# Optimization experiments

Hardware: AMD Instinct MI355X
Metric: run time of the kernel (lower is better)

## Reference

```python
import jax, jax.numpy as jnp
import numpy as np

B, T, C, H, MAX_LEN = 16, 512, 1024, 16, 512
D = C // H  # head_dim = 64

def setup_inputs() -> dict:
    key = jax.random.key(0)
    ks = jax.random.split(key, 10)
    s = 1.0 / np.sqrt(C)
    return {
        "x": jax.random.normal(ks[0], (B, T, C), dtype=jnp.float32),
        "Wq": jax.random.normal(ks[1], (C, C), dtype=jnp.float32) * s,
        "bq": jnp.zeros((C,), dtype=jnp.float32),
        "Wk": jax.random.normal(ks[2], (C, C), dtype=jnp.float32) * s,
        "bk": jnp.zeros((C,), dtype=jnp.float32),
        "Wv": jax.random.normal(ks[3], (C, C), dtype=jnp.float32) * s,
        "bv": jnp.zeros((C,), dtype=jnp.float32),
        "Wo": jax.random.normal(ks[4], (C, C), dtype=jnp.float32) * s,
        "bo": jnp.zeros((C,), dtype=jnp.float32),
        "rel_pos_bias": jax.random.normal(ks[5], (H, MAX_LEN, MAX_LEN), dtype=jnp.float32) * 0.02,
    }

def reference(x, Wq, bq, Wk, bk, Wv, bv, Wo, bo, rel_pos_bias):
    scale = 1.0 / jnp.sqrt(jnp.float32(D))
    # projections (torch Linear: x @ W.T + b), reshape to (B,H,T,D)
    def proj(W, b):
        return (x @ W.T + b).reshape(B, T, H, D).transpose(0, 2, 1, 3)
    q, k, v = proj(Wq, bq), proj(Wk, bk), proj(Wv, bv)
    attn = jnp.einsum('bhtd,bhsd->bhts', q, k) * scale  # (B,H,T,T)
    attn = attn + rel_pos_bias[None, :, :T, :T]
    causal = jnp.triu(jnp.ones((T, T), dtype=bool), k=1)
    attn = jnp.where(causal[None, None], -jnp.inf, attn)
    attn = jax.nn.softmax(attn, axis=-1)  # dropout p=0 (eval) -> identity
    out = jnp.einsum('bhts,bhsd->bhtd', attn, v)
    out = out.transpose(0, 2, 1, 3).reshape(B, T, C)
    return out @ Wo.T + bo
```

## Files before the change

### kernel.cpp

```cpp
#include <hip/hip_runtime.h>
#include <stdint.h>
#include <math.h>

#define DEV static __device__ __forceinline__

typedef __attribute__((ext_vector_type(8))) __bf16 bf16x8;
typedef __attribute__((ext_vector_type(4))) float f32x4;
typedef unsigned short u16;

DEV u16 f2b(float f) {
  union { float f; uint32_t u; } x; x.f = f;
  uint32_t r = x.u + 0x7fffu + ((x.u >> 16) & 1u);
  return (u16)(r >> 16);
}

DEV uint32_t pk2(float a, float b) {
  return (uint32_t)f2b(a) | ((uint32_t)f2b(b) << 16);
}

DEV float b2f_lo(uint32_t u) { return __uint_as_float(u << 16); }
DEV float b2f_hi(uint32_t u) { return __uint_as_float(u & 0xffff0000u); }

DEV void glds16(const void* g, void* l) {
  __builtin_amdgcn_global_load_lds(
      (const __attribute__((address_space(1))) void*)g,
      (__attribute__((address_space(3))) void*)l, 16, 0, 0);
}

DEV f32x4 mfma16(bf16x8 a, bf16x8 b, f32x4 c) {
  return __builtin_amdgcn_mfma_f32_16x16x32_bf16(a, b, c, 0, 0, 0);
}

__global__ __launch_bounds__(256) void cvt_all(
    const float* __restrict__ x, const float* __restrict__ Wq,
    const float* __restrict__ Wk, const float* __restrict__ Wv,
    const float* __restrict__ Wo, const float* __restrict__ bias,
    u16* __restrict__ xb, u16* __restrict__ wqkv, u16* __restrict__ wo,
    u16* __restrict__ biasb) {
  size_t i = ((size_t)blockIdx.x * 256 + threadIdx.x) * 4;
  const float* s;
  u16* d;
  size_t off;
  float scale = 1.0f;
  if (i < 8388608)        { s = x;  d = xb;             off = i; }
  else if (i < 9437184)   { s = Wq; d = wqkv;           off = i - 8388608; }
  else if (i < 10485760)  { s = Wk; d = wqkv + 1048576; off = i - 9437184; }
  else if (i < 11534336)  { s = Wv; d = wqkv + 2097152; off = i - 10485760; }
  else if (i < 12582912)  { s = Wo; d = wo;             off = i - 11534336; }
  else { s = bias; d = biasb; off = i - 12582912; scale = 1.44269504f; }
  float4 v = *(const float4*)(s + off);
  ushort4 o;
  o.x = f2b(v.x * scale); o.y = f2b(v.y * scale);
  o.z = f2b(v.z * scale); o.w = f2b(v.w * scale);
  *(ushort4*)(d + off) = o;
}

__global__ __launch_bounds__(256) void gemm_qkv(
    const u16* __restrict__ A, const u16* __restrict__ Bw,
    const float* __restrict__ bq, const float* __restrict__ bk,
    const float* __restrict__ bv,
    u16* __restrict__ qo, u16* __restrict__ ko, u16* __restrict__ vto) {
  __shared__ u16 lsA[2][128 * 32];
  __shared__ u16 lsB[2][128 * 32];
  const int K = 1024;
  int tid = threadIdx.x, wave = tid >> 6, lane = tid & 63;
  int q16 = lane >> 4, c16 = lane & 15;
  int m0 = blockIdx.y * 128, n0 = blockIdx.x * 128;
  int wm = wave >> 1, wn = wave & 1;
  const bool vblk = (n0 >= 2048);
  const u16* lsR = vblk ? &lsB[0][0] : &lsA[0][0];
  const u16* lsC = vblk ? &lsA[0][0] : &lsB[0][0];
  int wr = vblk ? wn : wm;
  int wc = vblk ? wm : wn;

  f32x4 acc[4][4];
#pragma unroll
  for (int i = 0; i < 4; ++i)
#pragma unroll
    for (int j = 0; j < 4; ++j) acc[i][j] = (f32x4)0.0f;

  int srow = (lane >> 2);
  int scol = ((lane & 3) ^ ((lane >> 3) & 3)) * 8;
  int swz = (q16 ^ ((c16 >> 1) & 3)) * 8;

  for (int k0 = 0; k0 < K; k0 += 64) {
    __syncthreads();
#pragma unroll
    for (int half = 0; half < 2; ++half) {
#pragma unroll
      for (int cc = 0; cc < 2; ++cc) {
        int chunk = wave * 2 + cc;
        int r = chunk * 16 + srow;
        glds16(A + (size_t)(m0 + r) * K + k0 + half * 32 + scol,
               &lsA[half][chunk * 512]);
        glds16(Bw + (size_t)(n0 + r) * K + k0 + half * 32 + scol,
               &lsB[half][chunk * 512]);
      }
    }
    __syncthreads();
#pragma unroll
    for (int half = 0; half < 2; ++half) {
      bf16x8 rf[4], cf[4];
#pragma unroll
      for (int i = 0; i < 4; ++i)
        rf[i] = *(const bf16x8*)&lsR[half * 4096 +
                                     (wr * 64 + i * 16 + c16) * 32 + swz];
#pragma unroll
      for (int i = 0; i < 4; ++i)
        cf[i] = *(const bf16x8*)&lsC[half * 4096 +
                                     (wc * 64 + i * 16 + c16) * 32 + swz];
#pragma unroll
      for (int it = 0; it < 4; ++it)
#pragma unroll
        for (int jt = 0; jt < 4; ++jt)
          acc[it][jt] = mfma16(rf[it], cf[jt], acc[it][jt]);
    }
  }

  if (!vblk) {
#pragma unroll
    for (int mt = 0; mt < 4; ++mt) {
#pragma unroll
      for (int nt = 0; nt < 4; ++nt) {
        int n = n0 + wn * 64 + nt * 16 + c16;
        int which = n >> 10;
        int nl = n & 1023;
        int hh = nl >> 6, d = nl & 63;
        float bias = (which == 0 ? bq : bk)[nl];
        u16* dst = (which == 0 ? qo : ko);
#pragma unroll
        for (int r = 0; r < 4; ++r) {
          int m = m0 + wm * 64 + mt * 16 + q16 * 4 + r;
          int b = m >> 9, t = m & 511;
          size_t bh = (size_t)b * 16 + hh;
          dst[(bh * 512 + t) * 72 + d] = f2b(acc[mt][nt][r] + bias);
        }
      }
    }
  } else {
#pragma unroll
    for (int it = 0; it < 4; ++it) {
      int nbase = n0 + wn * 64 + it * 16 + q16 * 4;
      float4 bvv = *(const float4*)(bv + (nbase & 1023));
#pragma unroll
      for (int jt = 0; jt < 4; ++jt) {
        int m = m0 + wm * 64 + jt * 16 + c16;
        int b = m >> 9, t = m & 511;
        size_t bh4 = ((size_t)b * 16) * 4;
#pragma unroll
        for (int r = 0; r < 4; ++r) {
          int nl = (nbase + r) & 1023;
          int hh = nl >> 6, d = nl & 63;
          float bias = ((const float*)&bvv)[r];
          vto[((bh4 + (size_t)hh * 4 + (t >> 7)) * 64 + d) * 136 + (t & 127)] =
              f2b(acc[it][jt][r] + bias);
        }
      }
    }
  }
}

__global__ __launch_bounds__(256, 3) void attn_kernel(
    const u16* __restrict__ qglob, const u16* __restrict__ kglob,
    const u16* __restrict__ vtglob, const u16* __restrict__ biasb,
    u16* __restrict__ og) {
  __shared__ u16 lsK[128 * 72];
  __shared__ u16 lsV[64 * 136];
  __shared__ u16 lsP[4 * 32 * 72];

  int tid = threadIdx.x, wave = tid >> 6, lane = tid & 63;
  int q16 = lane >> 4, c16 = lane & 15;
  int bh = blockIdx.y;
  int b = bh >> 4, h = bh & 15;
  int bx = blockIdx.x;
  int q0 = bx * 128;

  const u16* qbase = qglob + (size_t)bh * (512 * 72) + (size_t)q0 * 72;
  const u16* kbase = kglob + (size_t)bh * (512 * 72);
  const u16* vbase = vtglob + (size_t)bh * 4 * (64 * 136);
  u16* lsPw = lsP + wave * (32 * 72);

  for (int i = wave; i < 18; i += 4)
    glds16(qbase + (size_t)i * 512 + lane * 8, lsK + i * 512);
  __syncthreads();
  bf16x8 qf[2][2];
#pragma unroll
  for (int nt = 0; nt < 2; ++nt)
#pragma unroll
    for (int ks = 0; ks < 2; ++ks)
      qf[nt][ks] = *(const bf16x8*)&lsK[(wave * 32 + nt * 16 + c16) * 72 +
                                        ks * 32 + q16 * 8];

  f32x4 oacc[2][4];
#pragma unroll
  for (int i = 0; i < 2; ++i)
#pragma unroll
    for (int j = 0; j < 4; ++j) oacc[i][j] = (f32x4)0.0f;
  float mold[2] = {-INFINITY, -INFINITY};
  float lsum[2] = {0.0f, 0.0f};
  const float SCL = 0.18033688f;

  for (int st = 0; st <= bx; ++st) {
    bool diag = (st == bx);
    __syncthreads();
    const u16* kt = kbase + (size_t)st * (128 * 72);
    for (int i = wave; i < 18; i += 4)
      glds16(kt + (size_t)i * 512 + lane * 8, lsK + i * 512);
    const u16* vt = vbase + (size_t)st * (64 * 136);
    for (int i = wave; i < 17; i += 4)
      glds16(vt + (size_t)i * 512 + lane * 8, lsV + i * 512);

    uint2 ub[2][8];
#pragma unroll
    for (int nt = 0; nt < 2; ++nt) {
      int qgl = q0 + wave * 32 + nt * 16 + c16;
      const u16* bp = biasb + ((size_t)h * 512 + qgl) * 512 + st * 128 + q16 * 4;
#pragma unroll
      for (int mt = 0; mt < 8; ++mt) ub[nt][mt] = *(const uint2*)(bp + mt * 16);
    }
    __syncthreads();

    f32x4 sa[8][2];
#pragma unroll
    for (int mt = 0; mt < 8; ++mt) {
      sa[mt][0] = (f32x4)0.0f;
      sa[mt][1] = (f32x4)0.0f;
    }
    int mtmax = diag ? 2 * wave + 2 : 8;
#pragma unroll
    for (int mt = 0; mt < 8; ++mt) {
      if (mt < mtmax) {
#pragma unroll
        for (int ks = 0; ks < 2; ++ks) {
          bf16x8 kf =
              *(const bf16x8*)&lsK[(mt * 16 + c16) * 72 + ks * 32 + q16 * 8];
          sa[mt][0] = mfma16(kf, qf[0][ks], sa[mt][0]);
          sa[mt][1] = mfma16(kf, qf[1][ks], sa[mt][1]);
        }
      }
    }

    float alpha[2];
#pragma unroll
    for (int nt = 0; nt < 2; ++nt) {
#pragma unroll
      for (int mt = 0; mt < 8; ++mt) {
        uint32_t lo = ub[nt][mt].x, hi = ub[nt][mt].y;
        f32x4 bv;
        bv[0] = b2f_lo(lo); bv[1] = b2f_hi(lo);
        bv[2] = b2f_lo(hi); bv[3] = b2f_hi(hi);
        sa[mt][nt] = sa[mt][nt] * SCL + bv;
      }
      if (diag) {
#pragma unroll
        for (int mt = 0; mt < 8; ++mt) {
          int d0 = mt * 16 + q16 * 4 - wave * 32 - nt * 16 - c16;
#pragma unroll
          for (int r = 0; r < 4; ++r)
            if (d0 + r > 0) sa[mt][nt][r] = -INFINITY;
        }
      }
      f32x4 m4 = sa[0][nt];
#pragma unroll
      for (int mt = 1; mt < 8; ++mt) {
        f32x4 v = sa[mt][nt];
        m4[0] = fmaxf(m4[0], v[0]); m4[1] = fmaxf(m4[1], v[1]);
        m4[2] = fmaxf(m4[2], v[2]); m4[3] = fmaxf(m4[3], v[3]);
      }
      float mx = fmaxf(fmaxf(m4[0], m4[1]), fmaxf(m4[2], m4[3]));
      mx = fmaxf(mx, __shfl_xor(mx, 16));
      mx = fmaxf(mx, __shfl_xor(mx, 32));
      float mnew = fmaxf(mold[nt], mx);
      alpha[nt] = exp2f(mold[nt] - mnew);
      mold[nt] = mnew;
      f32x4 s4 = (f32x4)0.0f;
#pragma unroll
      for (int mt = 0; mt < 8; ++mt) {
        f32x4 p;
        p[0] = exp2f(sa[mt][nt][0] - mnew);
        p[1] = exp2f(sa[mt][nt][1] - mnew);
        p[2] = exp2f(sa[mt][nt][2] - mnew);
        p[3] = exp2f(sa[mt][nt][3] - mnew);
        sa[mt][nt] = p;
        s4 += p;
      }
      float ss = (s4[0] + s4[1]) + (s4[2] + s4[3]);
      ss += __shfl_xor(ss, 16);
      ss += __shfl_xor(ss, 32);
      lsum[nt] = lsum[nt] * alpha[nt] + ss;
    }

#pragma unroll
    for (int mo = 0; mo < 2; ++mo) {
      f32x4 av;
#pragma unroll
      for (int r = 0; r < 4; ++r) av[r] = __shfl(alpha[mo], q16 * 4 + r);
#pragma unroll
      for (int dt = 0; dt < 4; ++dt) oacc[mo][dt] *= av;
    }

    int G = diag ? wave + 1 : 4;
#pragma unroll
    for (int hf = 0; hf < 2; ++hf) {
      if (hf * 2 < G) {
#pragma unroll
        for (int nt = 0; nt < 2; ++nt)
#pragma unroll
          for (int mt4 = 0; mt4 < 4; ++mt4) {
            f32x4 p = sa[hf * 4 + mt4][nt];
            uint2 w;
            w.x = pk2(p[0], p[1]);
            w.y = pk2(p[2], p[3]);
            *(uint2*)&lsPw[(nt * 16 + c16) * 72 + mt4 * 16 + q16 * 4] = w;
          }
#pragma unroll
        for (int ksh = 0; ksh < 2; ++ksh) {
          if (hf * 2 + ksh < G) {
            bf16x8 pf0 =
                *(const bf16x8*)&lsPw[c16 * 72 + ksh * 32 + q16 * 8];
            bf16x8 pf1 =
                *(const bf16x8*)&lsPw[(16 + c16) * 72 + ksh * 32 + q16 * 8];
#pragma unroll
            for (int dt = 0; dt < 4; ++dt) {
              bf16x8 vf = *(const bf16x8*)&lsV[(dt * 16 + c16) * 136 +
                                               hf * 64 + ksh * 32 + q16 * 8];
              oacc[0][dt] = mfma16(pf0, vf, oacc[0][dt]);
              oacc[1][dt] = mfma16(pf1, vf, oacc[1][dt]);
            }
          }
        }
      }
    }
  }

#pragma unroll
  for (int mo = 0; mo < 2; ++mo) {
    f32x4 lv;
#pragma unroll
    for (int r = 0; r < 4; ++r) lv[r] = __shfl(lsum[mo], q16 * 4 + r);
#pragma unroll
    for (int r = 0; r < 4; ++r) {
      int tg = q0 + wave * 32 + mo * 16 + q16 * 4 + r;
      float inv = 1.0f / lv[r];
#pragma unroll
      for (int dt = 0; dt < 4; ++dt)
        og[((size_t)b * 512 + tg) * 1024 + h * 64 + dt * 16 + c16] =
            f2b(oacc[mo][dt][r] * inv);
    }
  }
}

__global__ __launch_bounds__(256) void gemm_out(
    const u16* __restrict__ A, const u16* __restrict__ W,
    const float* __restrict__ bo, float* __restrict__ out) {
  __shared__ u16 lsA[2][128 * 32];
  __shared__ u16 lsB[2][128 * 32];
  const int K = 1024;
  int tid = threadIdx.x, wave = tid >> 6, lane = tid & 63;
  int q16 = lane >> 4, c16 = lane & 15;
  int m0 = blockIdx.y * 128, n0 = blockIdx.x * 128;
  int wm = wave >> 1, wn = wave & 1;

  f32x4 acc[4][4];
#pragma unroll
  for (int i = 0; i < 4; ++i)
#pragma unroll
    for (int j = 0; j < 4; ++j) acc[i][j] = (f32x4)0.0f;

  int srow = (lane >> 2);
  int scol = ((lane & 3) ^ ((lane >> 3) & 3)) * 8;
  int swz = (q16 ^ ((c16 >> 1) & 3)) * 8;

  for (int k0 = 0; k0 < K; k0 += 64) {
    __syncthreads();
#pragma unroll
    for (int half = 0; half < 2; ++half) {
#pragma unroll
      for (int cc = 0; cc < 2; ++cc) {
        int chunk = wave * 2 + cc;
        int r = chunk * 16 + srow;
        glds16(A + (size_t)(m0 + r) * K + k0 + half * 32 + scol,
               &lsA[half][chunk * 512]);
        glds16(W + (size_t)(n0 + r) * K + k0 + half * 32 + scol,
               &lsB[half][chunk * 512]);
      }
    }
    __syncthreads();
#pragma unroll
    for (int half = 0; half < 2; ++half) {
      bf16x8 af[4], bf[4];
#pragma unroll
      for (int i = 0; i < 4; ++i)
        af[i] = *(const bf16x8*)&lsA[half][(wm * 64 + i * 16 + c16) * 32 + swz];
#pragma unroll
      for (int i = 0; i < 4; ++i)
        bf[i] = *(const bf16x8*)&lsB[half][(wn * 64 + i * 16 + c16) * 32 + swz];
#pragma unroll
      for (int mt = 0; mt < 4; ++mt)
#pragma unroll
        for (int nt = 0; nt < 4; ++nt)
          acc[mt][nt] = mfma16(af[mt], bf[nt], acc[mt][nt]);
    }
  }

#pragma unroll
  for (int mt = 0; mt < 4; ++mt) {
#pragma unroll
    for (int nt = 0; nt < 4; ++nt) {
      int n = n0 + wn * 64 + nt * 16 + c16;
      float bias = bo[n];
#pragma unroll
      for (int r = 0; r < 4; ++r) {
        int m = m0 + wm * 64 + mt * 16 + q16 * 4 + r;
        out[(size_t)m * 1024 + n] = acc[mt][nt][r] + bias;
      }
    }
  }
}

extern "C" void kernel_launch(void* const* d_in, const int* in_sizes, int n_in,
                              void* d_out, int out_size, void* d_ws, size_t ws_size,
                              hipStream_t stream) {
  const float* x    = (const float*)d_in[0];
  const float* Wq   = (const float*)d_in[1];
  const float* bq   = (const float*)d_in[2];
  const float* Wk   = (const float*)d_in[3];
  const float* bk   = (const float*)d_in[4];
  const float* Wv   = (const float*)d_in[5];
  const float* bv   = (const float*)d_in[6];
  const float* Wo   = (const float*)d_in[7];
  const float* bo   = (const float*)d_in[8];
  const float* bias = (const float*)d_in[9];
  float* out = (float*)d_out;

  const size_t MB = 1u << 20;
  char* ws = (char*)d_ws;
  u16* xb    = (u16*)(ws);
  u16* wqkv  = (u16*)(ws + 16 * MB);
  u16* wo    = (u16*)(ws + 22 * MB);
  u16* biasb = (u16*)(ws + 24 * MB);
  u16* qb    = (u16*)(ws + 32 * MB);
  u16* kb    = (u16*)(ws + 50 * MB);
  u16* vtb   = (u16*)(ws + 68 * MB);
  u16* ab    = xb;

  cvt_all<<<16384, 256, 0, stream>>>(x, Wq, Wk, Wv, Wo, bias,
                                     xb, wqkv, wo, biasb);
  gemm_qkv<<<dim3(24, 64), 256, 0, stream>>>(xb, wqkv, bq, bk, bv, qb, kb, vtb);
  attn_kernel<<<dim3(4, 256), 256, 0, stream>>>(qb, kb, vtb, biasb, ab);
  gemm_out<<<dim3(8, 64), 256, 0, stream>>>(ab, wo, bo, out);
}
```

Baseline: 289.5 us.

## Pair causal attention query tiles per block to balance work

The attention launch now uses a 1D grid of 640 blocks in place of 4x256. Blocks handling the longest query tile (4 KV steps) run alone, while the cheaper tiles are paired inside one block: tile 2 with tile 0, and two tile-1 jobs from adjacent heads. Each block then does about 4 KV steps of work. This targets the tail imbalance of causal attention. The cost is fewer blocks, serialized work within a block, and an extra barrier between the two jobs.

```diff
diff --git a/kernel.cpp b/kernel.cpp
--- a/kernel.cpp
+++ b/kernel.cpp
@@ -170,183 +170,195 @@
 
   int tid = threadIdx.x, wave = tid >> 6, lane = tid & 63;
   int q16 = lane >> 4, c16 = lane & 15;
-  int bh = blockIdx.y;
-  int b = bh >> 4, h = bh & 15;
-  int bx = blockIdx.x;
-  int q0 = bx * 128;
-
-  const u16* qbase = qglob + (size_t)bh * (512 * 72) + (size_t)q0 * 72;
-  const u16* kbase = kglob + (size_t)bh * (512 * 72);
-  const u16* vbase = vtglob + (size_t)bh * 4 * (64 * 136);
   u16* lsPw = lsP + wave * (32 * 72);
 
-  for (int i = wave; i < 18; i += 4)
-    glds16(qbase + (size_t)i * 512 + lane * 8, lsK + i * 512);
-  __syncthreads();
-  bf16x8 qf[2][2];
-#pragma unroll
-  for (int nt = 0; nt < 2; ++nt)
-#pragma unroll
-    for (int ks = 0; ks < 2; ++ks)
-      qf[nt][ks] = *(const bf16x8*)&lsK[(wave * 32 + nt * 16 + c16) * 72 +
-                                        ks * 32 + q16 * 8];
-
-  f32x4 oacc[2][4];
-#pragma unroll
-  for (int i = 0; i < 2; ++i)
-#pragma unroll
-    for (int j = 0; j < 4; ++j) oacc[i][j] = (f32x4)0.0f;
-  float mold[2] = {-INFINITY, -INFINITY};
-  float lsum[2] = {0.0f, 0.0f};
-  const float SCL = 0.18033688f;
-
-  for (int st = 0; st <= bx; ++st) {
-    bool diag = (st == bx);
-    __syncthreads();
-    const u16* kt = kbase + (size_t)st * (128 * 72);
+  int p = blockIdx.x;
+  int bx, bh, bx2 = -1, bh2 = 0;
+  if (p < 256)      { bx = 3; bh = p; }
+  else if (p < 512) { bx = 2; bh = p - 256; bx2 = 0; bh2 = p - 256; }
+  else              { int q = p - 512; bx = 1; bh = 2 * q; bx2 = 1; bh2 = 2 * q + 1; }
+
+  for (;;) {
+    int b = bh >> 4, h = bh & 15;
+    int q0 = bx * 128;
+
+    const u16* qbase = qglob + (size_t)bh * (512 * 72) + (size_t)q0 * 72;
+    const u16* kbase = kglob + (size_t)bh * (512 * 72);
+    const u16* vbase = vtglob + (size_t)bh * 4 * (64 * 136);
+
     for (int i = wave; i < 18; i += 4)
-      glds16(kt + (size_t)i * 512 + lane * 8, lsK + i * 512);
-    const u16* vt = vbase + (size_t)st * (64 * 136);
-    for (int i = wave; i < 17; i += 4)
-      glds16(vt + (size_t)i * 512 + lane * 8, lsV + i * 512);
-
-    uint2 ub[2][8];
-#pragma unroll
-    for (int nt = 0; nt < 2; ++nt) {
-      int qgl = q0 + wave * 32 + nt * 16 + c16;
-      const u16* bp = biasb + ((size_t)h * 512 + qgl) * 512 + st * 128 + q16 * 4;
-#pragma unroll
-      for (int mt = 0; mt < 8; ++mt) ub[nt][mt] = *(const uint2*)(bp + mt * 16);
-    }
-    __syncthreads();
-
-    f32x4 sa[8][2];
-#pragma unroll
-    for (int mt = 0; mt < 8; ++mt) {
-      sa[mt][0] = (f32x4)0.0f;
-      sa[mt][1] = (f32x4)0.0f;
-    }
-    int mtmax = diag ? 2 * wave + 2 : 8;
-#pragma unroll
-    for (int mt = 0; mt < 8; ++mt) {
-      if (mt < mtmax) {
-#pragma unroll
-        for (int ks = 0; ks < 2; ++ks) {
-          bf16x8 kf =
-              *(const bf16x8*)&lsK[(mt * 16 + c16) * 72 + ks * 32 + q16 * 8];
-          sa[mt][0] = mfma16(kf, qf[0][ks], sa[mt][0]);
-          sa[mt][1] = mfma16(kf, qf[1][ks], sa[mt][1]);
-        }
-      }
-    }
-
-    float alpha[2];
-#pragma unroll
-    for (int nt = 0; nt < 2; ++nt) {
+      glds16(qbase + (size_t)i * 512 + lane * 8, lsK + i * 512);
+    __syncthreads();
+    bf16x8 qf[2][2];
+#pragma unroll
+    for (int nt = 0; nt < 2; ++nt)
+#pragma unroll
+      for (int ks = 0; ks < 2; ++ks)
+        qf[nt][ks] = *(const bf16x8*)&lsK[(wave * 32 + nt * 16 + c16) * 72 +
+                                          ks * 32 + q16 * 8];
+
+    f32x4 oacc[2][4];
+#pragma unroll
+    for (int i = 0; i < 2; ++i)
+#pragma unroll
+      for (int j = 0; j < 4; ++j) oacc[i][j] = (f32x4)0.0f;
+    float mold[2] = {-INFINITY, -INFINITY};
+    float lsum[2] = {0.0f, 0.0f};
+    const float SCL = 0.18033688f;
+
+    for (int st = 0; st <= bx; ++st) {
+      bool diag = (st == bx);
+      __syncthreads();
+      const u16* kt = kbase + (size_t)st * (128 * 72);
+      for (int i = wave; i < 18; i += 4)
+        glds16(kt + (size_t)i * 512 + lane * 8, lsK + i * 512);
+      const u16* vt = vbase + (size_t)st * (64 * 136);
+      for (int i = wave; i < 17; i += 4)
+        glds16(vt + (size_t)i * 512 + lane * 8, lsV + i * 512);
+
+      uint2 ub[2][8];
+#pragma unroll
+      for (int nt = 0; nt < 2; ++nt) {
+        int qgl = q0 + wave * 32 + nt * 16 + c16;
+        const u16* bp =
+            biasb + ((size_t)h * 512 + qgl) * 512 + st * 128 + q16 * 4;
+#pragma unroll
+        for (int mt = 0; mt < 8; ++mt) ub[nt][mt] = *(const uint2*)(bp + mt * 16);
+      }
+      __syncthreads();
+
+      f32x4 sa[8][2];
 #pragma unroll
       for (int mt = 0; mt < 8; ++mt) {
-        uint32_t lo = ub[nt][mt].x, hi = ub[nt][mt].y;
-        f32x4 bv;
-        bv[0] = b2f_lo(lo); bv[1] = b2f_hi(lo);
-        bv[2] = b2f_lo(hi); bv[3] = b2f_hi(hi);
-        sa[mt][nt] = sa[mt][nt] * SCL + bv;
-      }
-      if (diag) {
+        sa[mt][0] = (f32x4)0.0f;
+        sa[mt][1] = (f32x4)0.0f;
+      }
+      int mtmax = diag ? 2 * wave + 2 : 8;
+#pragma unroll
+      for (int mt = 0; mt < 8; ++mt) {
+        if (mt < mtmax) {
+#pragma unroll
+          for (int ks = 0; ks < 2; ++ks) {
+            bf16x8 kf =
+                *(const bf16x8*)&lsK[(mt * 16 + c16) * 72 + ks * 32 + q16 * 8];
+            sa[mt][0] = mfma16(kf, qf[0][ks], sa[mt][0]);
+            sa[mt][1] = mfma16(kf, qf[1][ks], sa[mt][1]);
+          }
+        }
+      }
+
+      float alpha[2];
+#pragma unroll
+      for (int nt = 0; nt < 2; ++nt) {
 #pragma unroll
         for (int mt = 0; mt < 8; ++mt) {
-          int d0 = mt * 16 + q16 * 4 - wave * 32 - nt * 16 - c16;
-#pragma unroll
-          for (int r = 0; r < 4; ++r)
-            if (d0 + r > 0) sa[mt][nt][r] = -INFINITY;
-        }
-      }
-      f32x4 m4 = sa[0][nt];
-#pragma unroll
-      for (int mt = 1; mt < 8; ++mt) {
-        f32x4 v = sa[mt][nt];
-        m4[0] = fmaxf(m4[0], v[0]); m4[1] = fmaxf(m4[1], v[1]);
-        m4[2] = fmaxf(m4[2], v[2]); m4[3] = fmaxf(m4[3], v[3]);
-      }
-      float mx = fmaxf(fmaxf(m4[0], m4[1]), fmaxf(m4[2], m4[3]));
-      mx = fmaxf(mx, __shfl_xor(mx, 16));
-      mx = fmaxf(mx, __shfl_xor(mx, 32));
-      float mnew = fmaxf(mold[nt], mx);
-      alpha[nt] = exp2f(mold[nt] - mnew);
-      mold[nt] = mnew;
-      f32x4 s4 = (f32x4)0.0f;
-#pragma unroll
-      for (int mt = 0; mt < 8; ++mt) {
-        f32x4 p;
-        p[0] = exp2f(sa[mt][nt][0] - mnew);
-        p[1] = exp2f(sa[mt][nt][1] - mnew);
-        p[2] = exp2f(sa[mt][nt][2] - mnew);
-        p[3] = exp2f(sa[mt][nt][3] - mnew);
-        sa[mt][nt] = p;
-        s4 += p;
-      }
-      float ss = (s4[0] + s4[1]) + (s4[2] + s4[3]);
-      ss += __shfl_xor(ss, 16);
-      ss += __shfl_xor(ss, 32);
-      lsum[nt] = lsum[nt] * alpha[nt] + ss;
-    }
-
-#pragma unroll
-    for (int mo = 0; mo < 2; ++mo) {
-      f32x4 av;
-#pragma unroll
-      for (int r = 0; r < 4; ++r) av[r] = __shfl(alpha[mo], q16 * 4 + r);
-#pragma unroll
-      for (int dt = 0; dt < 4; ++dt) oacc[mo][dt] *= av;
-    }
-
-    int G = diag ? wave + 1 : 4;
-#pragma unroll
-    for (int hf = 0; hf < 2; ++hf) {
-      if (hf * 2 < G) {
-#pragma unroll
-        for (int nt = 0; nt < 2; ++nt)
-#pragma unroll
-          for (int mt4 = 0; mt4 < 4; ++mt4) {
-            f32x4 p = sa[hf * 4 + mt4][nt];
-            uint2 w;
-            w.x = pk2(p[0], p[1]);
-            w.y = pk2(p[2], p[3]);
-            *(uint2*)&lsPw[(nt * 16 + c16) * 72 + mt4 * 16 + q16 * 4] = w;
+          uint32_t lo = ub[nt][mt].x, hi = ub[nt][mt].y;
+          f32x4 bv;
+          bv[0] = b2f_lo(lo); bv[1] = b2f_hi(lo);
+          bv[2] = b2f_lo(hi); bv[3] = b2f_hi(hi);
+          sa[mt][nt] = sa[mt][nt] * SCL + bv;
+        }
+        if (diag) {
+#pragma unroll
+          for (int mt = 0; mt < 8; ++mt) {
+            int d0 = mt * 16 + q16 * 4 - wave * 32 - nt * 16 - c16;
+#pragma unroll
+            for (int r = 0; r < 4; ++r)
+              if (d0 + r > 0) sa[mt][nt][r] = -INFINITY;
           }
-#pragma unroll
-        for (int ksh = 0; ksh < 2; ++ksh) {
-          if (hf * 2 + ksh < G) {
-            bf16x8 pf0 =
-                *(const bf16x8*)&lsPw[c16 * 72 + ksh * 32 + q16 * 8];
-            bf16x8 pf1 =
-                *(const bf16x8*)&lsPw[(16 + c16) * 72 + ksh * 32 + q16 * 8];
-#pragma unroll
-            for (int dt = 0; dt < 4; ++dt) {
-              bf16x8 vf = *(const bf16x8*)&lsV[(dt * 16 + c16) * 136 +
-                                               hf * 64 + ksh * 32 + q16 * 8];
-              oacc[0][dt] = mfma16(pf0, vf, oacc[0][dt]);
-              oacc[1][dt] = mfma16(pf1, vf, oacc[1][dt]);
+        }
+        f32x4 m4 = sa[0][nt];
+#pragma unroll
+        for (int mt = 1; mt < 8; ++mt) {
+          f32x4 v = sa[mt][nt];
+          m4[0] = fmaxf(m4[0], v[0]); m4[1] = fmaxf(m4[1], v[1]);
+          m4[2] = fmaxf(m4[2], v[2]); m4[3] = fmaxf(m4[3], v[3]);
+        }
+        float mx = fmaxf(fmaxf(m4[0], m4[1]), fmaxf(m4[2], m4[3]));
+        mx = fmaxf(mx, __shfl_xor(mx, 16));
+        mx = fmaxf(mx, __shfl_xor(mx, 32));
+        float mnew = fmaxf(mold[nt], mx);
+        alpha[nt] = exp2f(mold[nt] - mnew);
+        mold[nt] = mnew;
+        f32x4 s4 = (f32x4)0.0f;
+#pragma unroll
+        for (int mt = 0; mt < 8; ++mt) {
+          f32x4 pq;
+          pq[0] = exp2f(sa[mt][nt][0] - mnew);
+          pq[1] = exp2f(sa[mt][nt][1] - mnew);
+          pq[2] = exp2f(sa[mt][nt][2] - mnew);
+          pq[3] = exp2f(sa[mt][nt][3] - mnew);
+          sa[mt][nt] = pq;
+          s4 += pq;
+        }
+        float ss = (s4[0] + s4[1]) + (s4[2] + s4[3]);
+        ss += __shfl_xor(ss, 16);
+        ss += __shfl_xor(ss, 32);
+        lsum[nt] = lsum[nt] * alpha[nt] + ss;
+      }
+
+#pragma unroll
+      for (int mo = 0; mo < 2; ++mo) {
+        f32x4 av;
+#pragma unroll
+        for (int r = 0; r < 4; ++r) av[r] = __shfl(alpha[mo], q16 * 4 + r);
+#pragma unroll
+        for (int dt = 0; dt < 4; ++dt) oacc[mo][dt] *= av;
+      }
+
+      int G = diag ? wave + 1 : 4;
+#pragma unroll
+      for (int hf = 0; hf < 2; ++hf) {
+        if (hf * 2 < G) {
+#pragma unroll
+          for (int nt = 0; nt < 2; ++nt)
+#pragma unroll
+            for (int mt4 = 0; mt4 < 4; ++mt4) {
+              f32x4 pv = sa[hf * 4 + mt4][nt];
+              uint2 w;
+              w.x = pk2(pv[0], pv[1]);
+              w.y = pk2(pv[2], pv[3]);
+              *(uint2*)&lsPw[(nt * 16 + c16) * 72 + mt4 * 16 + q16 * 4] = w;
+            }
+#pragma unroll
+          for (int ksh = 0; ksh < 2; ++ksh) {
+            if (hf * 2 + ksh < G) {
+              bf16x8 pf0 =
+                  *(const bf16x8*)&lsPw[c16 * 72 + ksh * 32 + q16 * 8];
+              bf16x8 pf1 =
+                  *(const bf16x8*)&lsPw[(16 + c16) * 72 + ksh * 32 + q16 * 8];
+#pragma unroll
+              for (int dt = 0; dt < 4; ++dt) {
+                bf16x8 vf = *(const bf16x8*)&lsV[(dt * 16 + c16) * 136 +
+                                                 hf * 64 + ksh * 32 + q16 * 8];
+                oacc[0][dt] = mfma16(pf0, vf, oacc[0][dt]);
+                oacc[1][dt] = mfma16(pf1, vf, oacc[1][dt]);
+              }
             }
           }
         }
       }
     }
-  }
-
-#pragma unroll
-  for (int mo = 0; mo < 2; ++mo) {
-    f32x4 lv;
-#pragma unroll
-    for (int r = 0; r < 4; ++r) lv[r] = __shfl(lsum[mo], q16 * 4 + r);
-#pragma unroll
-    for (int r = 0; r < 4; ++r) {
-      int tg = q0 + wave * 32 + mo * 16 + q16 * 4 + r;
-      float inv = 1.0f / lv[r];
-#pragma unroll
-      for (int dt = 0; dt < 4; ++dt)
-        og[((size_t)b * 512 + tg) * 1024 + h * 64 + dt * 16 + c16] =
-            f2b(oacc[mo][dt][r] * inv);
-    }
+
+#pragma unroll
+    for (int mo = 0; mo < 2; ++mo) {
+      f32x4 lv;
+#pragma unroll
+      for (int r = 0; r < 4; ++r) lv[r] = __shfl(lsum[mo], q16 * 4 + r);
+#pragma unroll
+      for (int r = 0; r < 4; ++r) {
+        int tg = q0 + wave * 32 + mo * 16 + q16 * 4 + r;
+        float inv = 1.0f / lv[r];
+#pragma unroll
+        for (int dt = 0; dt < 4; ++dt)
+          og[((size_t)b * 512 + tg) * 1024 + h * 64 + dt * 16 + c16] =
+              f2b(oacc[mo][dt][r] * inv);
+      }
+    }
+
+    if (bx2 < 0) break;
+    __syncthreads();
+    bx = bx2; bh = bh2; bx2 = -1;
   }
 }
 
@@ -447,6 +459,6 @@
   cvt_all<<<16384, 256, 0, stream>>>(x, Wq, Wk, Wv, Wo, bias,
                                      xb, wqkv, wo, biasb);
   gemm_qkv<<<dim3(24, 64), 256, 0, stream>>>(xb, wqkv, bq, bk, bv, qb, kb, vtb);
-  attn_kernel<<<dim3(4, 256), 256, 0, stream>>>(qb, kb, vtb, biasb, ab);
+  attn_kernel<<<dim3(640), 256, 0, stream>>>(qb, kb, vtb, biasb, ab);
   gemm_out<<<dim3(8, 64), 256, 0, stream>>>(ab, wo, bo, out);
 }
```

Result: faster. 280.1 us (-3.2%).
